# Kernel optimization log

Hardware: AMD Instinct MI355X
Metric: run time of the kernel (lower is better)

Reference implementation:

```python
import jax, jax.numpy as jnp
import numpy as np

MIN = 1e-30
BLOCK = 64


def setup_inputs() -> dict:
    key = jax.random.key(0)
    ks = jax.random.split(key, 16)
    B, L, D, H, M, E, P, R = 4, 512, 768, 12, 48, 32, 512, 97
    inp = {
        "context": jax.random.normal(ks[0], (B, L, D), jnp.float32),
        "attention": jax.random.uniform(ks[1], (B, H, L, L), jnp.float32),
        "mention_map": jax.random.uniform(ks[2], (B, M, L), jnp.float32),
        "entity_map": jax.random.uniform(ks[3], (B, E, M), jnp.float32),
        "hts": jax.random.randint(ks[4], (B, P, 2), 0, E).astype(jnp.int64),
        "hW": jax.random.normal(ks[5], (D, D), jnp.float32) * 0.02,
        "hb": jnp.zeros((D,), jnp.float32),
        "tW": jax.random.normal(ks[6], (D, D), jnp.float32) * 0.02,
        "tb": jnp.zeros((D,), jnp.float32),
        "hcW": jax.random.normal(ks[7], (D, D), jnp.float32) * 0.02,
        "hcb": jnp.zeros((D,), jnp.float32),
        "tcW": jax.random.normal(ks[8], (D, D), jnp.float32) * 0.02,
        "tcb": jnp.zeros((D,), jnp.float32),
        "clasW": jax.random.normal(ks[9], (R, D * BLOCK), jnp.float32) * 0.02,
        "clasb": jnp.zeros((R,), jnp.float32),
    }
    return inp


def _group_bilinear(h, t, W, b):
    # h, t: [B, P, D]; grouped bilinear a la ATLOP: block-outer-product then linear
    B, P, D = h.shape
    nb = D // BLOCK
    h_ = h.reshape(B, P, nb, BLOCK)
    t_ = t.reshape(B, P, nb, BLOCK)
    feat = jnp.einsum("bpni,bpnj->bpnij", h_, t_).reshape(B, P, D * BLOCK)
    return feat @ W.T + b


def _forward(context, attention, mention_map, entity_map, hts,
             hW, hb, tW, tb, hcW, hcb, tcW, tcb, clasW, clasb):
    B = context.shape[0]
    bidx = jnp.arange(B)[:, None]
    h_idx = hts[..., 0]  # [B, P]
    t_idx = hts[..., 1]
    ht_mask = (hts.sum(-1) != 0)[..., None].astype(context.dtype)  # [B, P, 1]

    # ---- get_ht ----
    mention = mention_map @ context                       # [B, M, D]
    att_sum = attention.sum(axis=1)                       # [B, L, L]
    mention_att = mention_map @ att_sum @ jnp.swapaxes(mention_map, 1, 2)  # [B, M, M]
    entity_att = entity_map @ mention_att                 # [B, E, M]

    h_mask = entity_map[bidx, h_idx] * ht_mask            # [B, P, M]
    t_mask = entity_map[bidx, t_idx] * ht_mask
    h_att = entity_att[bidx, h_idx] * t_mask
    t_att = entity_att[bidx, t_idx] * h_mask
    h_att = h_att / (h_att.sum(-1, keepdims=True) + MIN)
    t_att = t_att / (t_att.sum(-1, keepdims=True) + MIN)
    h = (t_att @ mention) * ht_mask                       # [B, P, D]
    t = (h_att @ mention) * ht_mask

    # ---- context_pooling (entity_map projected to token space) ----
    em_tok = entity_map @ mention_map                     # [B, E, L]
    em_tok = em_tok / (em_tok.sum(-1, keepdims=True) + MIN)
    ent_att = jnp.einsum("bel,bhlm->bhem", em_tok, attention)  # [B, H, E, L]
    hA = ent_att[bidx, :, h_idx]                          # [B, P, H, L]
    tA = ent_att[bidx, :, t_idx]
    ctx_att = (hA * tA).sum(axis=2)                       # [B, P, L]
    ctx_att = ctx_att / (ctx_att.sum(-1, keepdims=True) + MIN)
    context_info = (ctx_att @ context) * ht_mask          # [B, P, D]

    h_info = context_info @ hcW.T + hcb
    t_info = context_info @ tcW.T + tcb
    h = jnp.tanh(h @ hW.T + hb + h_info)
    t = jnp.tanh(t @ tW.T + tb + t_info)
    return _group_bilinear(h, t, clasW, clasb)            # [B, P, R]


def reference(context, attention, mention_map, entity_map, hts,
              hW, hb, tW, tb, hcW, hcb, tcW, tcb, clasW, clasb):
    return _forward(context, attention, mention_map, entity_map, hts,
                    hW, hb, tW, tb, hcW, hcb, tcW, tcb, clasW, clasb)
```

## Files before the change

kernel.cpp:

```cpp
#include <hip/hip_runtime.h>
#include <math.h>

#define Bc 4
#define Lc 512
#define Dc 768
#define Hc 12
#define Mc 48
#define Ec 32
#define Pc 512
#define Rc 97
#define MINV 1e-30f
#define NSLICE 24

typedef _Float16 f16;
typedef __attribute__((ext_vector_type(8))) _Float16 f16x8;
typedef __attribute__((ext_vector_type(4))) _Float16 f16x4;
typedef __attribute__((ext_vector_type(16))) float f32x16;

__global__ __launch_bounds__(256) void k_prep(const float* __restrict__ hW, const float* __restrict__ tW,
                                              const float* __restrict__ hcW, const float* __restrict__ tcW,
                                              f16* __restrict__ hWb, f16* __restrict__ tWb,
                                              f16* __restrict__ hcWb, f16* __restrict__ tcWb,
                                              const float* __restrict__ clasW, f16* __restrict__ Wp,
                                              const float* __restrict__ ctx, f16* __restrict__ ctxT,
                                              const float* __restrict__ mm, f16* __restrict__ mmH,
                                              const float* __restrict__ em, f16* __restrict__ emtH) {
    __shared__ f16 Ts[64][72];
    __shared__ float rowS[Mc];
    __shared__ float red[256];
    __shared__ float inv;
    int bid = blockIdx.x;
    int tid = threadIdx.x;
    if (bid < 2048) {
        const int DD = Dc * Dc;
        int i = bid * 256 + tid;
        int stride = 2048 * 256;
        for (; i < 4 * DD; i += stride) {
            int sel = i / DD, j = i % DD;
            const float* s = (sel == 0) ? hW : (sel == 1) ? tW : (sel == 2) ? hcW : tcW;
            f16* d = (sel == 0) ? hWb : (sel == 1) ? tWb : (sel == 2) ? hcWb : tcWb;
            d[j] = (f16)s[j];
        }
    } else if (bid < 5120) {
        int gid = (bid - 2048) * 256 + tid;
        int lane = gid & 63; int f = gid >> 6;
        int rt = f & 3; int s = (f >> 2) & 3; int c = f >> 4;
        int n_l = lane & 31, kg = lane >> 5;
        int r = rt * 32 + n_l;
        f16x8 v;
        if (r < Rc) {
            const float* src = clasW + (size_t)r * (Dc * 64) + c * 64 + s * 16 + kg * 8;
#pragma unroll
            for (int j = 0; j < 8; ++j) v[j] = (f16)src[j];
        } else {
#pragma unroll
            for (int j = 0; j < 8; ++j) v[j] = (f16)0.f;
        }
        ((f16x8*)Wp)[gid] = v;
    } else if (bid < 5504) {
        int id = bid - 5120;
        int dt = id % 12; int lt = (id / 12) % 8; int b = id / 96;
        int l0 = lt * 64, d0 = dt * 64;
        int r = tid >> 2, cg = tid & 3;
        const float* src = ctx + ((size_t)b * Lc + l0 + r) * Dc + d0 + cg * 16;
#pragma unroll
        for (int u = 0; u < 4; ++u) {
            float4 v = ((const float4*)src)[u];
            Ts[cg * 16 + u * 4 + 0][r] = (f16)v.x;
            Ts[cg * 16 + u * 4 + 1][r] = (f16)v.y;
            Ts[cg * 16 + u * 4 + 2][r] = (f16)v.z;
            Ts[cg * 16 + u * 4 + 3][r] = (f16)v.w;
        }
        __syncthreads();
        int dr = tid >> 2, seg = tid & 3;
        f16* dst = ctxT + ((size_t)b * Dc + d0 + dr) * Lc + l0 + seg * 16;
        f16x8 o0, o1;
#pragma unroll
        for (int j = 0; j < 8; ++j) { o0[j] = Ts[dr][seg * 16 + j]; o1[j] = Ts[dr][seg * 16 + 8 + j]; }
        *(f16x8*)dst = o0;
        *(f16x8*)(dst + 8) = o1;
    } else if (bid < 5552) {
        int gid = (bid - 5504) * 256 + tid;
        const float4* src = (const float4*)(mm + (size_t)gid * 8);
        float4 v0 = src[0], v1 = src[1];
        f16x8 o;
        o[0] = (f16)v0.x; o[1] = (f16)v0.y; o[2] = (f16)v0.z; o[3] = (f16)v0.w;
        o[4] = (f16)v1.x; o[5] = (f16)v1.y; o[6] = (f16)v1.z; o[7] = (f16)v1.w;
        ((f16x8*)mmH)[gid] = o;
    } else {
        int be = bid - 5552; int b = be / Ec;
        if (tid < Mc) rowS[tid] = em[(size_t)be * Mc + tid];
        __syncthreads();
        float v0 = 0.f, v1 = 0.f;
        {
            const float* mb0 = mm + (size_t)b * Mc * Lc + tid;
            const float* mb1 = mm + (size_t)b * Mc * Lc + tid + 256;
            for (int m = 0; m < Mc; ++m) {
                v0 += rowS[m] * mb0[(size_t)m * Lc];
                v1 += rowS[m] * mb1[(size_t)m * Lc];
            }
        }
        red[tid] = v0 + v1;
        __syncthreads();
        for (int s = 128; s > 0; s >>= 1) { if (tid < s) red[tid] += red[tid + s]; __syncthreads(); }
        if (tid == 0) inv = 1.f / (red[0] + MINV);
        __syncthreads();
        emtH[(size_t)be * Lc + tid] = (f16)(v0 * inv);
        emtH[(size_t)be * Lc + tid + 256] = (f16)(v1 * inv);
    }
}

__global__ __launch_bounds__(256) void k_att_mention(const f16* __restrict__ mmH,
                                                     const f16* __restrict__ emtH,
                                                     const float* __restrict__ att,
                                                     float* __restrict__ tmpML,
                                                     float* __restrict__ eat,
                                                     const f16* __restrict__ ctxT,
                                                     float* __restrict__ mention) {
    __shared__ __align__(16) char smem[32768];
    int bid = blockIdx.x;
    int tid = threadIdx.x;
    int w = tid >> 6, lane = tid & 63;
    if (bid < 384) {
        f16* Ss   = (f16*)smem;
        f16* attS = (f16*)(smem + 12288);
        int mt = bid & 7; int bh = bid >> 3;
        int b = bh / Hc, h = bh % Hc;
        int m0 = mt * 64;
        int n_l = lane & 31, kg = lane >> 5;

        const float* ab = att + (size_t)bh * Lc * Lc + m0;
        int mRow = tid & 63, lg = tid >> 6;
        float pre[16];
#pragma unroll
        for (int q = 0; q < 16; ++q) pre[q] = ab[(size_t)(lg * 16 + q) * Lc + mRow];

        f32x16 acc[2];
#pragma unroll
        for (int nt = 0; nt < 2; ++nt)
#pragma unroll
            for (int i = 0; i < 16; ++i) acc[nt][i] = 0.f;

        for (int kc = 0; kc < 8; ++kc) {
            __syncthreads();
#pragma unroll
            for (int half = 0; half < 2; ++half) {
                int cc = lg * 2 + half;
                f16x8 v;
#pragma unroll
                for (int jj = 0; jj < 8; ++jj) v[jj] = (f16)pre[half * 8 + jj];
                ((f16x8*)attS)[mRow * 8 + (cc ^ (mRow & 7))] = v;
            }
#pragma unroll
            for (int k = 0; k < 3; ++k) {
                int idx = tid + k * 256;
                int row = idx >> 3, cc = idx & 7;
                f16x8 v;
                if (row < Mc) {
                    v = *(const f16x8*)(mmH + ((size_t)b * Mc + row) * Lc + kc * 64 + cc * 8);
                } else if (row < 80) {
                    v = *(const f16x8*)(emtH + ((size_t)b * Ec + row - Mc) * Lc + kc * 64 + cc * 8);
                } else {
#pragma unroll
                    for (int j = 0; j < 8; ++j) v[j] = (f16)0.f;
                }
                ((f16x8*)Ss)[row * 8 + (cc ^ (row & 7))] = v;
            }
            if (kc < 7) {
#pragma unroll
                for (int q = 0; q < 16; ++q)
                    pre[q] = ab[(size_t)((kc + 1) * 64 + lg * 16 + q) * Lc + mRow];
            }
            __syncthreads();
            if (w < 3) {
                int arow = w * 32 + n_l;
#pragma unroll
                for (int kk = 0; kk < 4; ++kk) {
                    int cc = kk * 2 + kg;
                    f16x8 a = ((const f16x8*)Ss)[arow * 8 + (cc ^ (arow & 7))];
#pragma unroll
                    for (int nt = 0; nt < 2; ++nt) {
                        int bcol = nt * 32 + n_l;
                        f16x8 bb = ((const f16x8*)attS)[bcol * 8 + (cc ^ (bcol & 7))];
                        acc[nt] = __builtin_amdgcn_mfma_f32_32x32x16_f16(a, bb, acc[nt], 0, 0, 0);
                    }
                }
            }
        }
        if (w < 3) {
#pragma unroll
            for (int nt = 0; nt < 2; ++nt)
#pragma unroll
                for (int reg = 0; reg < 16; ++reg) {
                    int row = (reg & 3) + 8 * (reg >> 2) + 4 * kg;
                    int rr = w * 32 + row;
                    int col = m0 + nt * 32 + n_l;
                    if (rr < Mc) {
                        atomicAdd(&tmpML[((size_t)b * Mc + rr) * Lc + col], acc[nt][reg]);
                    } else if (rr < 80) {
                        eat[(((size_t)b * Hc + h) * Ec + (rr - Mc)) * Lc + col] = acc[nt][reg];
                    }
                }
        }
    } else {
        f16* As = (f16*)smem;
        f16* Bs = (f16*)(smem + 16384);
        int id = bid - 384;
        int dt = id % 12; int b = id / 12;
        int d0 = dt * 64;
        int w_m = w & 1, w_n = w >> 1;
        int m_l = lane & 31, kg = lane >> 5;
        int r0 = tid >> 3, cc0 = tid & 7;
        int r1 = r0 + 32;
        int mr0 = (r0 < Mc) ? r0 : r0 - Mc;
        int mr1 = (r1 < Mc) ? r1 : r1 - Mc;
        f16x8 ar0, ar1, br0, br1;
        auto loadt = [&](int it) {
            int k0 = it * 64;
            ar0 = *(const f16x8*)(mmH + ((size_t)b * Mc + mr0) * Lc + k0 + cc0 * 8);
            ar1 = *(const f16x8*)(mmH + ((size_t)b * Mc + mr1) * Lc + k0 + cc0 * 8);
            br0 = *(const f16x8*)(ctxT + ((size_t)b * Dc + d0 + r0) * Lc + k0 + cc0 * 8);
            br1 = *(const f16x8*)(ctxT + ((size_t)b * Dc + d0 + r1) * Lc + k0 + cc0 * 8);
        };
        auto writet = [&](int p) {
            ((f16x8*)(As + p * 4096))[r0 * 8 + (cc0 ^ (r0 & 7))] = ar0;
            ((f16x8*)(As + p * 4096))[r1 * 8 + (cc0 ^ (r1 & 7))] = ar1;
            ((f16x8*)(Bs + p * 4096))[r0 * 8 + (cc0 ^ (r0 & 7))] = br0;
            ((f16x8*)(Bs + p * 4096))[r1 * 8 + (cc0 ^ (r1 & 7))] = br1;
        };
        loadt(0); writet(0); loadt(1);
        f32x16 acc;
#pragma unroll
        for (int i = 0; i < 16; ++i) acc[i] = 0.f;
        int ar = w_m * 32 + m_l;
        int br = w_n * 32 + m_l;
        for (int it = 0; it < 8; ++it) {
            int p = it & 1;
            __syncthreads();
            if (it < 7) writet(p ^ 1);
            if (it < 6) loadt(it + 2);
#pragma unroll
            for (int s = 0; s < 4; ++s) {
                int ck = s * 2 + kg;
                f16x8 a = ((const f16x8*)(As + p * 4096))[ar * 8 + (ck ^ (ar & 7))];
                f16x8 bv = ((const f16x8*)(Bs + p * 4096))[br * 8 + (ck ^ (br & 7))];
                acc = __builtin_amdgcn_mfma_f32_32x32x16_f16(a, bv, acc, 0, 0, 0);
            }
        }
#pragma unroll
        for (int reg = 0; reg < 16; ++reg) {
            int row = (reg & 3) + 8 * (reg >> 2) + 4 * kg;
            int m = w_m * 32 + row;
            if (m < Mc) mention[((size_t)b * Mc + m) * Dc + d0 + w_n * 32 + m_l] = acc[reg];
        }
    }
}

__global__ __launch_bounds__(256) void k_ma(const float* __restrict__ tmp,
                                            const float* __restrict__ mm,
                                            float* __restrict__ maS) {
    int wv = threadIdx.x >> 6, lane = threadIdx.x & 63;
    int gid = blockIdx.x * 4 + wv;
    int m2 = gid % 48;
    int m  = (gid / 48) % 48;
    int b  = gid / (48 * 48);
    const float4* t = (const float4*)(tmp + ((size_t)b * Mc + m)  * Lc);
    const float4* r = (const float4*)(mm  + ((size_t)b * Mc + m2) * Lc);
    float4 a0 = t[lane],      b0 = r[lane];
    float4 a1 = t[lane + 64], b1 = r[lane + 64];
    float acc = a0.x * b0.x + a0.y * b0.y + a0.z * b0.z + a0.w * b0.w
              + a1.x * b1.x + a1.y * b1.y + a1.z * b1.z + a1.w * b1.w;
#pragma unroll
    for (int off = 1; off < 64; off <<= 1) acc += __shfl_xor(acc, off);
    if (lane == 0) maS[gid] = acc;
}

__global__ __launch_bounds__(256) void k_ea(const float* __restrict__ maS,
                                            const float* __restrict__ em,
                                            float* __restrict__ ea) {
    __shared__ float S[48 * 48];
    int b  = blockIdx.x >> 3;
    int eg = blockIdx.x & 7;
    int tid = threadIdx.x;
    for (int i = tid; i < 48 * 48; i += 256) S[i] = maS[(size_t)b * 48 * 48 + i];
    __syncthreads();
    int wv = tid >> 6, lane = tid & 63;
    int e = eg * 4 + wv;
    if (lane < 48) {
        const float* emr = em + ((size_t)b * Ec + e) * Mc;
        float acc = 0.f;
#pragma unroll
        for (int m = 0; m < 48; ++m) acc += emr[m] * S[m * 48 + lane];
        ea[((size_t)b * Ec + e) * Mc + lane] = acc;
    }
}

__global__ __launch_bounds__(256) void k_pair(const int* __restrict__ hts,
                                              const float* __restrict__ em,
                                              const float* __restrict__ ea,
                                              const float* __restrict__ eat,
                                              f16* __restrict__ hatN, f16* __restrict__ tatN,
                                              f16* __restrict__ caH) {
    int wv = threadIdx.x >> 6, lane = threadIdx.x & 63;
    int bp = blockIdx.x * 4 + wv;
    int b = bp >> 9;
    int hi = hts[bp * 2], ti = hts[bp * 2 + 1];
    float mask = (hi + ti != 0) ? 1.f : 0.f;
    float hat = 0.f, tat = 0.f;
    if (lane < Mc) {
        float hm = em[((size_t)(b * Ec + hi)) * Mc + lane];
        float tm = em[((size_t)(b * Ec + ti)) * Mc + lane];
        float eh = ea[((size_t)(b * Ec + hi)) * Mc + lane];
        float et = ea[((size_t)(b * Ec + ti)) * Mc + lane];
        hat = eh * tm * mask;
        tat = et * hm * mask;
    }
    float sh = hat, st = tat;
#pragma unroll
    for (int off = 1; off < 64; off <<= 1) { sh += __shfl_xor(sh, off); st += __shfl_xor(st, off); }
    float hnorm = 1.f / (sh + MINV);
    float tnorm = 1.f / (st + MINV);
    hatN[(size_t)bp * 64 + lane] = (f16)(hat * hnorm);
    tatN[(size_t)bp * 64 + lane] = (f16)(tat * tnorm);

    const float* base = eat + (size_t)b * Hc * Ec * Lc;
    float prod[8];
    float tot = 0.f;
#pragma unroll
    for (int j8 = 0; j8 < 8; ++j8) {
        int j = j8 * 64 + lane;
        float a = 0.f;
#pragma unroll
        for (int h = 0; h < Hc; ++h)
            a += base[((size_t)h * Ec + hi) * Lc + j] * base[((size_t)h * Ec + ti) * Lc + j];
        prod[j8] = a;
        tot += a;
    }
#pragma unroll
    for (int off = 1; off < 64; off <<= 1) tot += __shfl_xor(tot, off);
    float inv = 1.f / (tot + MINV);
#pragma unroll
    for (int j8 = 0; j8 < 8; ++j8)
        caH[(size_t)bp * Lc + j8 * 64 + lane] = (f16)(prod[j8] * inv);
}

__global__ __launch_bounds__(256) void k_htci(const f16* __restrict__ tatN, const f16* __restrict__ hatN,
                                              const float* __restrict__ mention,
                                              f16* __restrict__ hB, f16* __restrict__ tB,
                                              const int* __restrict__ hts,
                                              const f16* __restrict__ caH,
                                              const f16* __restrict__ ctxT,
                                              f16* __restrict__ ci) {
    __shared__ __align__(16) char smem[33024];
    int bid = blockIdx.x;
    int tid = threadIdx.x;
    int w = tid >> 6, lane = tid & 63;
    int w_m = w & 1, w_n = w >> 1;
    int m_l = lane & 31, kg = lane >> 5;
    if (bid < 384) {
        f16* At = (f16*)smem;
        f16* Ah = (f16*)(smem + 8192);
        f16* Bs = (f16*)(smem + 16384);
        int m0 = (bid & 31) * 64;
        int b = m0 >> 9;
        int d0 = (bid >> 5) * 64;

        for (int i = tid; i < 512; i += 256) {
            int p = i >> 3, c = i & 7;
            ((f16x8*)At)[p * 8 + (c ^ (p & 7))] = *(const f16x8*)(tatN + (size_t)(m0 + p) * 64 + c * 8);
            ((f16x8*)Ah)[p * 8 + (c ^ (p & 7))] = *(const f16x8*)(hatN + (size_t)(m0 + p) * 64 + c * 8);
        }
        for (int i = tid; i < 512; i += 256) {
            f16x8 z;
#pragma unroll
            for (int j = 0; j < 8; ++j) z[j] = (f16)0.f;
            ((f16x8*)Bs)[i] = z;
        }
        __syncthreads();
        if (tid < 192) {
            int m = tid >> 2, q = tid & 3;
            const float4* src = (const float4*)(mention + ((size_t)b * Mc + m) * Dc + d0 + q * 16);
#pragma unroll
            for (int u = 0; u < 4; ++u) {
                float4 v = src[u];
                int dl = q * 16 + u * 4;
#pragma unroll
                for (int x = 0; x < 4; ++x) {
                    float vv = (x == 0) ? v.x : (x == 1) ? v.y : (x == 2) ? v.z : v.w;
                    int d = dl + x;
                    Bs[(d * 8 + ((m >> 3) ^ (d & 7))) * 8 + (m & 7)] = (f16)vv;
                }
            }
        }
        __syncthreads();

        f32x16 acch, acct;
#pragma unroll
        for (int i = 0; i < 16; ++i) { acch[i] = 0.f; acct[i] = 0.f; }
        int ar = w_m * 32 + m_l;
        int br = w_n * 32 + m_l;
#pragma unroll
        for (int s = 0; s < 4; ++s) {
            int ck = s * 2 + kg;
            f16x8 at_ = ((const f16x8*)At)[ar * 8 + (ck ^ (ar & 7))];
            f16x8 ah_ = ((const f16x8*)Ah)[ar * 8 + (ck ^ (ar & 7))];
            f16x8 bv = ((const f16x8*)Bs)[br * 8 + (ck ^ (br & 7))];
            acch = __builtin_amdgcn_mfma_f32_32x32x16_f16(at_, bv, acch, 0, 0, 0);
            acct = __builtin_amdgcn_mfma_f32_32x32x16_f16(ah_, bv, acct, 0, 0, 0);
        }
#pragma unroll
        for (int reg = 0; reg < 16; ++reg) {
            int row = (reg & 3) + 8 * (reg >> 2) + 4 * kg;
            int p = m0 + w_m * 32 + row;
            int d = d0 + w_n * 32 + m_l;
            hB[(size_t)p * Dc + d] = (f16)acch[reg];
            tB[(size_t)p * Dc + d] = (f16)acct[reg];
        }
    } else {
        f16* As = (f16*)smem;
        f16* Bs = (f16*)(smem + 16384);
        float* maskS = (float*)(smem + 32768);
        int id = bid - 384;
        int dt = id % 12; int pt = (id / 12) % 8; int b = id / 96;
        int p0 = pt * 64, d0 = dt * 64;
        int r0 = tid >> 3, cc0 = tid & 7;
        int r1 = r0 + 32;
        if (tid < 64) {
            int bp = b * Pc + p0 + tid;
            maskS[tid] = (hts[bp * 2] + hts[bp * 2 + 1] != 0) ? 1.f : 0.f;
        }
        f16x8 ar0, ar1, br0, br1;
        auto loadt = [&](int it) {
            int k0 = it * 64;
            ar0 = *(const f16x8*)(caH + (size_t)(b * Pc + p0 + r0) * Lc + k0 + cc0 * 8);
            ar1 = *(const f16x8*)(caH + (size_t)(b * Pc + p0 + r1) * Lc + k0 + cc0 * 8);
            br0 = *(const f16x8*)(ctxT + (size_t)(b * Dc + d0 + r0) * Lc + k0 + cc0 * 8);
            br1 = *(const f16x8*)(ctxT + (size_t)(b * Dc + d0 + r1) * Lc + k0 + cc0 * 8);
        };
        auto writet = [&](int p) {
            ((f16x8*)(As + p * 4096))[r0 * 8 + (cc0 ^ (r0 & 7))] = ar0;
            ((f16x8*)(As + p * 4096))[r1 * 8 + (cc0 ^ (r1 & 7))] = ar1;
            ((f16x8*)(Bs + p * 4096))[r0 * 8 + (cc0 ^ (r0 & 7))] = br0;
            ((f16x8*)(Bs + p * 4096))[r1 * 8 + (cc0 ^ (r1 & 7))] = br1;
        };
        loadt(0); writet(0); loadt(1);
        f32x16 acc;
#pragma unroll
        for (int i = 0; i < 16; ++i) acc[i] = 0.f;
        int ar = w_m * 32 + m_l;
        int br = w_n * 32 + m_l;
        for (int it = 0; it < 8; ++it) {
            int p = it & 1;
            __syncthreads();
            if (it < 7) writet(p ^ 1);
            if (it < 6) loadt(it + 2);
#pragma unroll
            for (int s = 0; s < 4; ++s) {
                int ck = s * 2 + kg;
                f16x8 a = ((const f16x8*)(As + p * 4096))[ar * 8 + (ck ^ (ar & 7))];
                f16x8 bv = ((const f16x8*)(Bs + p * 4096))[br * 8 + (ck ^ (br & 7))];
                acc = __builtin_amdgcn_mfma_f32_32x32x16_f16(a, bv, acc, 0, 0, 0);
            }
        }
#pragma unroll
        for (int reg = 0; reg < 16; ++reg) {
            int row = (reg & 3) + 8 * (reg >> 2) + 4 * kg;
            int p = p0 + w_m * 32 + row;
            int d = d0 + w_n * 32 + m_l;
            ci[(size_t)(b * Pc + p) * Dc + d] = (f16)(acc[reg] * maskS[w_m * 32 + row]);
        }
    }
}

__global__ __launch_bounds__(256) void k_proj_mfma(const f16* __restrict__ Xh, const f16* __restrict__ Wh,
                                                   const float* __restrict__ bh,
                                                   const f16* __restrict__ Xt, const f16* __restrict__ Wt,
                                                   const float* __restrict__ bt,
                                                   const f16* __restrict__ Xc, const f16* __restrict__ Whc,
                                                   const float* __restrict__ bhc,
                                                   const f16* __restrict__ Wtc, const float* __restrict__ btc,
                                                   f16* __restrict__ outh, f16* __restrict__ outt) {
    __shared__ __align__(16) f16 Xs[2][64 * 64];
    __shared__ __align__(16) f16 Ws[2][64 * 64];
    int z = blockIdx.z;
    const f16* X1 = z ? Xt : Xh;
    const f16* W1 = z ? Wt : Wh;
    const float* b1 = z ? bt : bh;
    const f16* W2 = z ? Wtc : Whc;
    const float* b2 = z ? btc : bhc;
    f16* outp = z ? outt : outh;
    int m0 = blockIdx.x * 64, n0 = blockIdx.y * 64;
    int tid = threadIdx.x;
    int w = tid >> 6, lane = tid & 63;
    int w_m = w & 1, w_n = w >> 1;
    int m_l = lane & 31, kg = lane >> 5;
    const f16* Xarr[2] = {X1, Xc};
    const f16* Warr[2] = {W1, W2};
    int r0 = tid >> 3, cc0 = tid & 7;
    int r1 = r0 + 32;
    f16x8 xr0, xr1, wr0, wr1;
    auto loadt = [&](int it) {
        int src = it / 12; int k0 = (it % 12) * 64;
        const f16* X = Xarr[src]; const f16* W = Warr[src];
        xr0 = *(const f16x8*)(X + (size_t)(m0 + r0) * Dc + k0 + cc0 * 8);
        xr1 = *(const f16x8*)(X + (size_t)(m0 + r1) * Dc + k0 + cc0 * 8);
        wr0 = *(const f16x8*)(W + (size_t)(n0 + r0) * Dc + k0 + cc0 * 8);
        wr1 = *(const f16x8*)(W + (size_t)(n0 + r1) * Dc + k0 + cc0 * 8);
    };
    auto writet = [&](int p) {
        ((f16x8*)Xs[p])[r0 * 8 + (cc0 ^ (r0 & 7))] = xr0;
        ((f16x8*)Xs[p])[r1 * 8 + (cc0 ^ (r1 & 7))] = xr1;
        ((f16x8*)Ws[p])[r0 * 8 + (cc0 ^ (r0 & 7))] = wr0;
        ((f16x8*)Ws[p])[r1 * 8 + (cc0 ^ (r1 & 7))] = wr1;
    };
    loadt(0); writet(0); loadt(1);
    f32x16 acc;
#pragma unroll
    for (int i = 0; i < 16; ++i) acc[i] = 0.f;
    int ar = w_m * 32 + m_l;
    int br = w_n * 32 + m_l;
    for (int it = 0; it < 24; ++it) {
        int p = it & 1;
        __syncthreads();
        if (it < 23) writet(p ^ 1);
        if (it < 22) loadt(it + 2);
#pragma unroll
        for (int s = 0; s < 4; ++s) {
            int ck = s * 2 + kg;
            f16x8 a = ((const f16x8*)Xs[p])[ar * 8 + (ck ^ (ar & 7))];
            f16x8 b = ((const f16x8*)Ws[p])[br * 8 + (ck ^ (br & 7))];
            acc = __builtin_amdgcn_mfma_f32_32x32x16_f16(a, b, acc, 0, 0, 0);
        }
    }
#pragma unroll
    for (int reg = 0; reg < 16; ++reg) {
        int row = (reg & 3) + 8 * (reg >> 2) + 4 * kg;
        int m = m0 + w_m * 32 + row;
        int n = n0 + w_n * 32 + m_l;
        float v = tanhf(acc[reg] + b1[n] + b2[n]);
        outp[(size_t)m * Dc + n] = (f16)v;
    }
}

__global__ __launch_bounds__(256, 3) void k_bilin(const f16* __restrict__ hF, const f16* __restrict__ tF,
                                                  const f16* __restrict__ Wp, f16* __restrict__ partial) {
    __shared__ __align__(16) f16 tS[128 * 64];
    __shared__ f16 hS[128 * 33];
    int id = blockIdx.x;
    int tile = id / NSLICE;
    int slice = id % NSLICE;
    int bp0 = tile * 128;
    int tid = threadIdx.x;
    int w = tid >> 6, lane = tid & 63;
    int w_m = w & 1, w_r = w >> 1;
    int m_l = lane & 31, kg = lane >> 5;
    int c0 = slice * 32;
    int n = c0 >> 6;

    for (int idx = tid; idx < 128 * 4; idx += 256) {
        int bp = idx >> 2, seg = idx & 3;
        f16x8 hv = *(const f16x8*)(hF + (size_t)(bp0 + bp) * Dc + c0 + seg * 8);
#pragma unroll
        for (int j = 0; j < 8; ++j) hS[bp * 33 + seg * 8 + j] = hv[j];
    }
    for (int idx = tid; idx < 128 * 8; idx += 256) {
        int bp = idx >> 3, cc = idx & 7;
        f16x8 tv = *(const f16x8*)(tF + (size_t)(bp0 + bp) * Dc + n * 64 + cc * 8);
        ((f16x8*)tS)[bp * 8 + (cc ^ (bp & 7))] = tv;
    }
    __syncthreads();

    f32x16 acc[2][2];
#pragma unroll
    for (int mt = 0; mt < 2; ++mt)
#pragma unroll
        for (int rt = 0; rt < 2; ++rt)
#pragma unroll
            for (int i = 0; i < 16; ++i) acc[mt][rt][i] = 0.f;

    int rowA = w_m * 64 + m_l;
    int rowB = rowA + 32;
    const f16x8* WpB = (const f16x8*)Wp;

    for (int ii = 0; ii < 32; ++ii) {
        int cc = c0 + ii;
        const f16x8* wpb = WpB + (size_t)cc * 16 * 64 + lane;
        f16x8 Bf[8];
#pragma unroll
        for (int s = 0; s < 4; ++s) {
            Bf[s * 2 + 0] = wpb[(s * 4 + 2 * w_r + 0) * 64];
            Bf[s * 2 + 1] = wpb[(s * 4 + 2 * w_r + 1) * 64];
        }
        f16 hv0 = hS[rowA * 33 + ii];
        f16 hv1 = hS[rowB * 33 + ii];
#pragma unroll
        for (int s = 0; s < 4; ++s) {
            int ck = s * 2 + kg;
            f16x8 tv0 = ((const f16x8*)tS)[rowA * 8 + (ck ^ (rowA & 7))];
            f16x8 tv1 = ((const f16x8*)tS)[rowB * 8 + (ck ^ (rowB & 7))];
            f16x8 a0 = tv0 * hv0;
            f16x8 a1 = tv1 * hv1;
            acc[0][0] = __builtin_amdgcn_mfma_f32_32x32x16_f16(a0, Bf[s * 2 + 0], acc[0][0], 0, 0, 0);
            acc[1][0] = __builtin_amdgcn_mfma_f32_32x32x16_f16(a1, Bf[s * 2 + 0], acc[1][0], 0, 0, 0);
            acc[0][1] = __builtin_amdgcn_mfma_f32_32x32x16_f16(a0, Bf[s * 2 + 1], acc[0][1], 0, 0, 0);
            acc[1][1] = __builtin_amdgcn_mfma_f32_32x32x16_f16(a1, Bf[s * 2 + 1], acc[1][1], 0, 0, 0);
        }
    }

    f16* pbase = partial + (size_t)slice * (2048 * 128);
#pragma unroll
    for (int rt = 0; rt < 2; ++rt) {
        int r = (w_r * 2 + rt) * 32 + m_l;
#pragma unroll
        for (int mt = 0; mt < 2; ++mt)
#pragma unroll
            for (int reg = 0; reg < 16; ++reg) {
                int row = (reg & 3) + 8 * (reg >> 2) + 4 * kg;
                int bp = bp0 + w_m * 64 + mt * 32 + row;
                pbase[(size_t)bp * 128 + r] = (f16)acc[mt][rt][reg];
            }
    }
}

__global__ __launch_bounds__(256) void k_reduce(const f16* __restrict__ partial,
                                                const float* __restrict__ cb,
                                                float* __restrict__ out) {
    int idx = blockIdx.x * 256 + threadIdx.x;
    int bp = idx >> 5, c = idx & 31;
    const f16x4* p = (const f16x4*)partial + idx;
    float a0 = 0.f, a1 = 0.f, a2 = 0.f, a3 = 0.f;
#pragma unroll
    for (int s = 0; s < NSLICE; ++s) {
        f16x4 v = p[(size_t)s * (2048 * 32)];
        a0 += (float)v[0]; a1 += (float)v[1]; a2 += (float)v[2]; a3 += (float)v[3];
    }
    int rb = c * 4;
    float* ob = out + (size_t)bp * Rc;
    if (rb + 0 < Rc) ob[rb + 0] = a0 + cb[rb + 0];
    if (rb + 1 < Rc) ob[rb + 1] = a1 + cb[rb + 1];
    if (rb + 2 < Rc) ob[rb + 2] = a2 + cb[rb + 2];
    if (rb + 3 < Rc) ob[rb + 3] = a3 + cb[rb + 3];
}

extern "C" void kernel_launch(void* const* d_in, const int* in_sizes, int n_in,
                              void* d_out, int out_size, void* d_ws, size_t ws_size,
                              hipStream_t stream) {
    const float* context   = (const float*)d_in[0];
    const float* attention = (const float*)d_in[1];
    const float* mm        = (const float*)d_in[2];
    const float* em        = (const float*)d_in[3];
    const int*   hts       = (const int*)d_in[4];
    const float* hW        = (const float*)d_in[5];
    const float* hb        = (const float*)d_in[6];
    const float* tW        = (const float*)d_in[7];
    const float* tb        = (const float*)d_in[8];
    const float* hcW       = (const float*)d_in[9];
    const float* hcb       = (const float*)d_in[10];
    const float* tcW       = (const float*)d_in[11];
    const float* tcb       = (const float*)d_in[12];
    const float* clasW     = (const float*)d_in[13];
    const float* clasb     = (const float*)d_in[14];
    float* out = (float*)d_out;

    char* wsb = (char*)d_ws;
    auto alloc = [&](size_t bytes) { char* p = wsb; wsb += (bytes + 255) & ~(size_t)255; return p; };
    float* mention     = (float*)alloc((size_t)Bc * Mc * Dc * 4);
    float* tmpML       = (float*)alloc((size_t)Bc * Mc * Lc * 4);
    float* entity_att  = (float*)alloc((size_t)Bc * Ec * Mc * 4);
    float* ent_att     = (float*)alloc((size_t)Bc * Hc * Ec * Lc * 4);
    float* maS         = (float*)alloc((size_t)Bc * Mc * Mc * 4);
    f16* em_tok  = (f16*)alloc((size_t)Bc * Ec * Lc * 2);
    f16* ctx_att = (f16*)alloc((size_t)Bc * Pc * Lc * 2);
    f16* mmH     = (f16*)alloc((size_t)Bc * Mc * Lc * 2);
    f16* hatN    = (f16*)alloc((size_t)Bc * Pc * 64 * 2);
    f16* tatN    = (f16*)alloc((size_t)Bc * Pc * 64 * 2);
    f16* h_buf   = (f16*)alloc((size_t)Bc * Pc * Dc * 2);
    f16* t_buf   = (f16*)alloc((size_t)Bc * Pc * Dc * 2);
    f16* ctxinfo = (f16*)alloc((size_t)Bc * Pc * Dc * 2);
    f16* h_fin   = (f16*)alloc((size_t)Bc * Pc * Dc * 2);
    f16* t_fin   = (f16*)alloc((size_t)Bc * Pc * Dc * 2);
    f16* hWb     = (f16*)alloc((size_t)Dc * Dc * 2);
    f16* tWb     = (f16*)alloc((size_t)Dc * Dc * 2);
    f16* hcWb    = (f16*)alloc((size_t)Dc * Dc * 2);
    f16* tcWb    = (f16*)alloc((size_t)Dc * Dc * 2);
    f16* ctxT    = (f16*)alloc((size_t)Bc * Dc * Lc * 2);
    f16* Wp      = (f16*)alloc((size_t)768 * 16 * 64 * 8 * 2);
    f16* partial = (f16*)alloc((size_t)NSLICE * 2048 * 128 * 2);

    hipMemsetAsync(tmpML, 0, (size_t)Bc * Mc * Lc * 4, stream);
    k_prep<<<dim3(5680), dim3(256), 0, stream>>>(hW, tW, hcW, tcW, hWb, tWb, hcWb, tcWb,
                                                 clasW, Wp, context, ctxT, mm, mmH, em, em_tok);
    k_att_mention<<<dim3(432), dim3(256), 0, stream>>>(mmH, em_tok, attention, tmpML, ent_att,
                                                       ctxT, mention);
    k_ma<<<dim3(Bc * Mc * Mc / 4), dim3(256), 0, stream>>>(tmpML, mm, maS);
    k_ea<<<dim3(Bc * 8), dim3(256), 0, stream>>>(maS, em, entity_att);
    k_pair<<<dim3(Bc * Pc / 4), dim3(256), 0, stream>>>(hts, em, entity_att, ent_att, hatN, tatN, ctx_att);
    k_htci<<<dim3(768), dim3(256), 0, stream>>>(tatN, hatN, mention, h_buf, t_buf,
                                                hts, ctx_att, ctxT, ctxinfo);
    k_proj_mfma<<<dim3(32, 12, 2), dim3(256), 0, stream>>>(h_buf, hWb, hb, t_buf, tWb, tb,
                                                           ctxinfo, hcWb, hcb, tcWb, tcb, h_fin, t_fin);
    k_bilin<<<dim3(16 * NSLICE), dim3(256), 0, stream>>>(h_fin, t_fin, Wp, partial);
    k_reduce<<<dim3(256), dim3(256), 0, stream>>>(partial, clasb, out);
}
```

Before: 265.3 us.

## Split bilinear kernel over relation halves with register-cached t fragments and B prefetch

```diff
diff --git a/kernel.cpp b/kernel.cpp
--- a/kernel.cpp
+++ b/kernel.cpp
@@ -547,15 +547,18 @@
     __shared__ __align__(16) f16 tS[128 * 64];
     __shared__ f16 hS[128 * 33];
     int id = blockIdx.x;
-    int tile = id / NSLICE;
-    int slice = id % NSLICE;
+    int rh = id & 1;
+    int st = id >> 1;
+    int slice = st % NSLICE;
+    int tile = st / NSLICE;
     int bp0 = tile * 128;
+    int c0 = slice * 32;
+    int n = c0 >> 6;
     int tid = threadIdx.x;
     int w = tid >> 6, lane = tid & 63;
     int w_m = w & 1, w_r = w >> 1;
     int m_l = lane & 31, kg = lane >> 5;
-    int c0 = slice * 32;
-    int n = c0 >> 6;
+    int rt = rh * 2 + w_r;
 
     for (int idx = tid; idx < 128 * 4; idx += 256) {
         int bp = idx >> 2, seg = idx & 3;
@@ -570,56 +573,69 @@
     }
     __syncthreads();
 
-    f32x16 acc[2][2];
-#pragma unroll
-    for (int mt = 0; mt < 2; ++mt)
-#pragma unroll
-        for (int rt = 0; rt < 2; ++rt)
-#pragma unroll
-            for (int i = 0; i < 16; ++i) acc[mt][rt][i] = 0.f;
-
     int rowA = w_m * 64 + m_l;
     int rowB = rowA + 32;
-    const f16x8* WpB = (const f16x8*)Wp;
-
-    for (int ii = 0; ii < 32; ++ii) {
-        int cc = c0 + ii;
-        const f16x8* wpb = WpB + (size_t)cc * 16 * 64 + lane;
-        f16x8 Bf[8];
-#pragma unroll
-        for (int s = 0; s < 4; ++s) {
-            Bf[s * 2 + 0] = wpb[(s * 4 + 2 * w_r + 0) * 64];
-            Bf[s * 2 + 1] = wpb[(s * 4 + 2 * w_r + 1) * 64];
-        }
-        f16 hv0 = hS[rowA * 33 + ii];
-        f16 hv1 = hS[rowB * 33 + ii];
-#pragma unroll
-        for (int s = 0; s < 4; ++s) {
-            int ck = s * 2 + kg;
-            f16x8 tv0 = ((const f16x8*)tS)[rowA * 8 + (ck ^ (rowA & 7))];
-            f16x8 tv1 = ((const f16x8*)tS)[rowB * 8 + (ck ^ (rowB & 7))];
-            f16x8 a0 = tv0 * hv0;
-            f16x8 a1 = tv1 * hv1;
-            acc[0][0] = __builtin_amdgcn_mfma_f32_32x32x16_f16(a0, Bf[s * 2 + 0], acc[0][0], 0, 0, 0);
-            acc[1][0] = __builtin_amdgcn_mfma_f32_32x32x16_f16(a1, Bf[s * 2 + 0], acc[1][0], 0, 0, 0);
-            acc[0][1] = __builtin_amdgcn_mfma_f32_32x32x16_f16(a0, Bf[s * 2 + 1], acc[0][1], 0, 0, 0);
-            acc[1][1] = __builtin_amdgcn_mfma_f32_32x32x16_f16(a1, Bf[s * 2 + 1], acc[1][1], 0, 0, 0);
+
+    f16x8 tvA[4], tvB[4];
+#pragma unroll
+    for (int s = 0; s < 4; ++s) {
+        int ck = s * 2 + kg;
+        tvA[s] = ((const f16x8*)tS)[rowA * 8 + (ck ^ (rowA & 7))];
+        tvB[s] = ((const f16x8*)tS)[rowB * 8 + (ck ^ (rowB & 7))];
+    }
+
+    f32x16 acc[2];
+#pragma unroll
+    for (int mt = 0; mt < 2; ++mt)
+#pragma unroll
+        for (int i = 0; i < 16; ++i) acc[mt][i] = 0.f;
+
+    const f16x8* wpb = (const f16x8*)Wp + ((size_t)c0 * 16 + rt) * 64 + lane;
+    f16x8 BfA[4], BfB[4];
+#pragma unroll
+    for (int s = 0; s < 4; ++s) BfA[s] = wpb[s * 256];
+
+    for (int io = 0; io < 32; io += 2) {
+#pragma unroll
+        for (int s = 0; s < 4; ++s) BfB[s] = wpb[(io + 1) * 1024 + s * 256];
+        {
+            f16 hv0 = hS[rowA * 33 + io];
+            f16 hv1 = hS[rowB * 33 + io];
+#pragma unroll
+            for (int s = 0; s < 4; ++s) {
+                f16x8 a0 = tvA[s] * hv0;
+                f16x8 a1 = tvB[s] * hv1;
+                acc[0] = __builtin_amdgcn_mfma_f32_32x32x16_f16(a0, BfA[s], acc[0], 0, 0, 0);
+                acc[1] = __builtin_amdgcn_mfma_f32_32x32x16_f16(a1, BfA[s], acc[1], 0, 0, 0);
+            }
+        }
+        if (io + 2 < 32) {
+#pragma unroll
+            for (int s = 0; s < 4; ++s) BfA[s] = wpb[(io + 2) * 1024 + s * 256];
+        }
+        {
+            f16 hv0 = hS[rowA * 33 + io + 1];
+            f16 hv1 = hS[rowB * 33 + io + 1];
+#pragma unroll
+            for (int s = 0; s < 4; ++s) {
+                f16x8 a0 = tvA[s] * hv0;
+                f16x8 a1 = tvB[s] * hv1;
+                acc[0] = __builtin_amdgcn_mfma_f32_32x32x16_f16(a0, BfB[s], acc[0], 0, 0, 0);
+                acc[1] = __builtin_amdgcn_mfma_f32_32x32x16_f16(a1, BfB[s], acc[1], 0, 0, 0);
+            }
         }
     }
 
     f16* pbase = partial + (size_t)slice * (2048 * 128);
-#pragma unroll
-    for (int rt = 0; rt < 2; ++rt) {
-        int r = (w_r * 2 + rt) * 32 + m_l;
-#pragma unroll
-        for (int mt = 0; mt < 2; ++mt)
-#pragma unroll
-            for (int reg = 0; reg < 16; ++reg) {
-                int row = (reg & 3) + 8 * (reg >> 2) + 4 * kg;
-                int bp = bp0 + w_m * 64 + mt * 32 + row;
-                pbase[(size_t)bp * 128 + r] = (f16)acc[mt][rt][reg];
-            }
-    }
+    int r = rt * 32 + m_l;
+#pragma unroll
+    for (int mt = 0; mt < 2; ++mt)
+#pragma unroll
+        for (int reg = 0; reg < 16; ++reg) {
+            int row = (reg & 3) + 8 * (reg >> 2) + 4 * kg;
+            int bp = bp0 + w_m * 64 + mt * 32 + row;
+            pbase[(size_t)bp * 128 + r] = (f16)acc[mt][reg];
+        }
 }
 
 __global__ __launch_bounds__(256) void k_reduce(const f16* __restrict__ partial,
@@ -699,6 +715,6 @@
                                                 hts, ctx_att, ctxT, ctxinfo);
     k_proj_mfma<<<dim3(32, 12, 2), dim3(256), 0, stream>>>(h_buf, hWb, hb, t_buf, tWb, tb,
                                                            ctxinfo, hcWb, hcb, tcWb, tcb, h_fin, t_fin);
-    k_bilin<<<dim3(16 * NSLICE), dim3(256), 0, stream>>>(h_fin, t_fin, Wp, partial);
+    k_bilin<<<dim3(16 * NSLICE * 2), dim3(256), 0, stream>>>(h_fin, t_fin, Wp, partial);
     k_reduce<<<dim3(256), dim3(256), 0, stream>>>(partial, clasb, out);
 }
```

Result: faster. 247.0 us (-6.9%).
